# Kernel tuning notes

Measured on AMD Instinct MI355X. Metric: run time of the kernel, lower is better.

The kernel has to match this reference:

```python
import jax, jax.numpy as jnp
import numpy as np

N = 50000
E = 800000
NODE_DIM = 15
HID = 64
HEADS = 4
NEG_SLOPE = 0.2


def _add_self_loops(edge_index, n):
    loops = jnp.arange(n, dtype=edge_index.dtype)
    src = jnp.concatenate([edge_index[0], loops])
    dst = jnp.concatenate([edge_index[1], loops])
    return src, dst


def gat_conv(x, edge_index, W, att_src, att_dst, bias, concat):
    # x: [N, F_in]; W: [F_in, heads*out]; att_*: [heads, out]; bias: [heads*out] or [out]
    n = x.shape[0]
    heads, out_dim = att_src.shape
    src, dst = _add_self_loops(edge_index, n)
    h = (x @ W).reshape(n, heads, out_dim)              # [N, H, D]
    a_src = jnp.sum(h * att_src[None], axis=-1)          # [N, H]
    a_dst = jnp.sum(h * att_dst[None], axis=-1)          # [N, H]
    e = a_src[src] + a_dst[dst]                          # [E', H]
    e = jnp.where(e > 0, e, NEG_SLOPE * e)               # LeakyReLU(0.2)
    # segment softmax over incoming edges of each dst node
    m = jax.ops.segment_max(e, dst, num_segments=n)      # [N, H]
    m = jnp.where(jnp.isfinite(m), m, 0.0)
    w = jnp.exp(e - m[dst])                              # [E', H]
    z = jax.ops.segment_sum(w, dst, num_segments=n)      # [N, H]
    alpha = w / z[dst]                                   # [E', H]
    msg = alpha[:, :, None] * h[src]                     # [E', H, D]
    out = jax.ops.segment_sum(msg, dst, num_segments=n)  # [N, H, D]
    if concat:
        return out.reshape(n, heads * out_dim) + bias
    return out.mean(axis=1) + bias


def setup_inputs() -> dict:
    key = jax.random.key(0)
    ks = jax.random.split(key, 11)
    x = jax.random.normal(ks[0], (N, NODE_DIM), dtype=jnp.float32)
    edge_index = jax.random.randint(ks[1], (2, E), 0, N, dtype=jnp.int64)
    s1 = 1.0 / np.sqrt(NODE_DIM)
    s2 = 1.0 / np.sqrt(HEADS * HID)
    return {
        "x": x,
        "edge_index": edge_index,
        "W1": jax.random.normal(ks[2], (NODE_DIM, HEADS * HID), dtype=jnp.float32) * s1,
        "att_src1": jax.random.normal(ks[3], (HEADS, HID), dtype=jnp.float32) * s2,
        "att_dst1": jax.random.normal(ks[4], (HEADS, HID), dtype=jnp.float32) * s2,
        "b1": jnp.zeros((HEADS * HID,), dtype=jnp.float32),
        "W2": jax.random.normal(ks[5], (HEADS * HID, HID), dtype=jnp.float32) * s2,
        "att_src2": jax.random.normal(ks[6], (1, HID), dtype=jnp.float32) * s2,
        "att_dst2": jax.random.normal(ks[7], (1, HID), dtype=jnp.float32) * s2,
        "b2": jnp.zeros((HID,), dtype=jnp.float32),
    }


def reference(x, edge_index, W1, att_src1, att_dst1, b1, W2, att_src2, att_dst2, b2):
    h = gat_conv(x, edge_index, W1, att_src1, att_dst1, b1, concat=True)   # [N, 256]
    h = jax.nn.elu(h)
    # dropout p=0.2 skipped (eval mode)
    h = gat_conv(h, edge_index, W2, att_src2, att_dst2, b2, concat=True)   # heads=1 -> [N, 64]
    return h.mean(axis=0)                                                   # [64]
```

## Files before the change

kernel.cpp:

```cpp
#include <hip/hip_runtime.h>
#include <hip/hip_fp16.h>

#define NNODES 50000
#define NEDGES 800000
#define NEG_SLOPE 0.2f
#define NTOT (NEDGES + NNODES)
#define NB_NODE ((NNODES + 255) / 256)
#define CHUNK 4096
#define NCHUNK ((NEDGES + CHUNK - 1) / CHUNK)
#define CAPB 4800
#define CNTSTRIDE 16
#define ZPAD (NTOT + 32)

typedef _Float16 half8 __attribute__((ext_vector_type(8)));
typedef _Float16 half4 __attribute__((ext_vector_type(4)));
typedef float f32x4 __attribute__((ext_vector_type(4)));

__global__ void setup_scatter(const float* __restrict__ x, const float* __restrict__ W1,
                              const float* __restrict__ att_src, const float* __restrict__ att_dst,
                              const float* __restrict__ W2,
                              const int* __restrict__ srcs, const int* __restrict__ dsts,
                              int* __restrict__ bucket_cnt, int* __restrict__ bucketbuf,
                              float* __restrict__ x16, float* __restrict__ asrc4,
                              float* __restrict__ adst4, _Float16* __restrict__ W2T) {
    int t = threadIdx.x;
    __shared__ unsigned short meta[CHUNK];
    __shared__ int lcnt[NB_NODE], lbase[NB_NODE];
    __shared__ float swa[16][4], swd[16][4];
    if (blockIdx.x < NCHUNK) {
        int b = blockIdx.x;
        for (int i = t; i < NB_NODE; i += 256) lcnt[i] = 0;
        __syncthreads();
        int e0 = b * CHUNK;
        int e1 = e0 + CHUNK; if (e1 > NEDGES) e1 = NEDGES;
        for (int e = e0 + t; e < e1; e += 256) {
            int d = dsts[e];
            meta[e - e0] = (unsigned short)d;
            atomicAdd(&lcnt[d >> 8], 1);
        }
        __syncthreads();
        for (int i = t; i < NB_NODE; i += 256) {
            int c = lcnt[i];
            lbase[i] = c ? atomicAdd(&bucket_cnt[i * CNTSTRIDE], c) : 0;
        }
        __syncthreads();
        for (int i = t; i < NB_NODE; i += 256) lcnt[i] = 0;
        __syncthreads();
        for (int e = e0 + t; e < e1; e += 256) {
            int dv = meta[e - e0];
            int bk = dv >> 8;
            int pos = lbase[bk] + atomicAdd(&lcnt[bk], 1);
            if (pos < CAPB) bucketbuf[bk * CAPB + pos] = ((dv & 255) << 16) | srcs[e];
        }
    } else {
        int b = blockIdx.x - NCHUNK;
        if (t < 128) {
            int k = (t & 63) >> 2, h = t & 3;
            float s = 0.f;
            if (k < 15) {
                const float* att = (t < 64) ? att_src : att_dst;
#pragma unroll 16
                for (int d = 0; d < 64; ++d)
                    s += W1[k * 256 + h * 64 + d] * att[h * 64 + d];
            }
            if (t < 64) swa[k][h] = s; else swd[k][h] = s;
        }
        int tid = b * 256 + t;
        if (tid < 64 * 256) {
            int n = tid >> 8, k = tid & 255;
            W2T[n * 256 + k] = (_Float16)W2[k * 64 + n];
        }
        __syncthreads();
        int nid = tid;
        if (nid < NNODES) {
            float xv[16];
#pragma unroll
            for (int k = 0; k < 15; ++k) xv[k] = x[nid * 15 + k];
            xv[15] = 0.f;
#pragma unroll
            for (int k = 0; k < 16; k += 4)
                *(float4*)(x16 + (size_t)nid * 16 + k) =
                    make_float4(xv[k], xv[k+1], xv[k+2], xv[k+3]);
            float ps[4] = {0.f, 0.f, 0.f, 0.f}, pd[4] = {0.f, 0.f, 0.f, 0.f};
#pragma unroll
            for (int k = 0; k < 15; ++k)
#pragma unroll
                for (int h = 0; h < 4; ++h) {
                    ps[h] += xv[k] * swa[k][h];
                    pd[h] += xv[k] * swd[k][h];
                }
            *(float4*)(asrc4 + nid * 4) = make_float4(ps[0], ps[1], ps[2], ps[3]);
            *(float4*)(adst4 + nid * 4) = make_float4(pd[0], pd[1], pd[2], pd[3]);
        }
    }
}

__global__ void scanA(const int* __restrict__ bucket_cnt, const int* __restrict__ bucketbuf,
                      int* __restrict__ rowstart, int* __restrict__ partials) {
    int b = blockIdx.x, t = threadIdx.x, lane = t & 63, wid = t >> 6;
    __shared__ int hist[256];
    __shared__ int ws[4];
    int i = b * 256 + t;
    hist[t] = (i < NNODES) ? 1 : 0;
    __syncthreads();
    int n = bucket_cnt[b * CNTSTRIDE]; if (n > CAPB) n = CAPB;
    const int* buf = bucketbuf + (size_t)b * CAPB;
    for (int j = t; j < n; j += 256)
        atomicAdd(&hist[buf[j] >> 16], 1);
    __syncthreads();
    int v = (i < NNODES) ? hist[t] : 0;
    int incl = v;
#pragma unroll
    for (int off = 1; off < 64; off <<= 1) {
        int u = __shfl_up(incl, off, 64);
        if (lane >= off) incl += u;
    }
    if (lane == 63) ws[wid] = incl;
    __syncthreads();
    int w0 = ws[0], w1 = ws[1], w2 = ws[2], w3 = ws[3];
    int woff = (wid > 0 ? w0 : 0) + (wid > 1 ? w1 : 0) + (wid > 2 ? w2 : 0);
    if (i < NNODES) rowstart[i] = woff + (incl - v);
    if (t == 0) partials[b] = w0 + w1 + w2 + w3;
}

__global__ void scanB(const int* __restrict__ partials, int* __restrict__ blockoff,
                      int* __restrict__ rowstart, int nb) {
    int t = threadIdx.x, lane = t & 63, wid = t >> 6;
    int v = (t < nb) ? partials[t] : 0;
    int incl = v;
#pragma unroll
    for (int off = 1; off < 64; off <<= 1) {
        int u = __shfl_up(incl, off, 64);
        if (lane >= off) incl += u;
    }
    __shared__ int ws[4];
    if (lane == 63) ws[wid] = incl;
    __syncthreads();
    int w0 = ws[0], w1 = ws[1], w2 = ws[2], w3 = ws[3];
    int woff = (wid > 0 ? w0 : 0) + (wid > 1 ? w1 : 0) + (wid > 2 ? w2 : 0);
    if (t < nb) blockoff[t] = woff + (incl - v);
    if (t == 0) rowstart[NNODES] = w0 + w1 + w2 + w3;
}

__global__ void local_sort(const int* __restrict__ bucket_cnt, const int* __restrict__ bucketbuf,
                           int* __restrict__ rowstart, const int* __restrict__ blockoff,
                           const int* __restrict__ partials,
                           const float4* __restrict__ asrc4, const float4* __restrict__ adst4,
                           int* __restrict__ srclist, float4* __restrict__ sw4) {
    int b = blockIdx.x, t = threadIdx.x;
    __shared__ int cur[256];
    __shared__ int local[8192];
    __shared__ float4 sadst[256];
    if (b == 0 && t == 0) sw4[ZPAD] = make_float4(0.f, 0.f, 0.f, 0.f);
    int boff = blockoff[b];
    int base = rowstart[b * 256] + boff;
    int idx = b * 256 + t;
    int fin = (idx < NNODES) ? rowstart[idx] + boff : 0;
    cur[t] = (idx < NNODES) ? (fin - base) : 0;
    int nid = idx;
    if (nid < NNODES) sadst[t] = adst4[nid];
    __syncthreads();
    if (nid < NNODES) rowstart[nid] = fin;
    if (nid < NNODES) {
        int pos = atomicAdd(&cur[t], 1);
        local[pos] = (t << 16) | nid;
    }
    int n = bucket_cnt[b * CNTSTRIDE]; if (n > CAPB) n = CAPB;
    const int* buf = bucketbuf + (size_t)b * CAPB;
    for (int i = t; i < n; i += 256) {
        int entry = buf[i];
        int pos = atomicAdd(&cur[entry >> 16], 1);
        local[pos] = entry;
    }
    __syncthreads();
    int total = partials[b];
    for (int i = t; i < total; i += 256) {
        int e = local[i];
        int s = e & 0xFFFF, dl = e >> 16;
        srclist[base + i] = s;
        float4 as = asrc4[s];
        float4 ad = sadst[dl];
        float e0 = as.x + ad.x, e1 = as.y + ad.y, e2 = as.z + ad.z, e3 = as.w + ad.w;
        e0 = fmaxf(e0, NEG_SLOPE * e0); e1 = fmaxf(e1, NEG_SLOPE * e1);
        e2 = fmaxf(e2, NEG_SLOPE * e2); e3 = fmaxf(e3, NEG_SLOPE * e3);
        sw4[base + i] = make_float4(__expf(e0), __expf(e1), __expf(e2), __expf(e3));
    }
}

__global__ void layer1_aggr(const float* __restrict__ x16, const int* __restrict__ rowstart,
                            const int* __restrict__ srclist, const float4* __restrict__ sw4,
                            const float* __restrict__ W1, const float* __restrict__ b1,
                            __half* __restrict__ out1) {
    int wid = threadIdx.x >> 6, lane = threadIdx.x & 63;
    int g = lane >> 4, k = lane & 15;
    int base = blockIdx.x * 16 + wid * 4;
    int nid = base + g;
    int beg = rowstart[nid];
    int cnt = rowstart[nid + 1] - beg;
    int cmax = cnt;
    cmax = max(cmax, __shfl_xor(cmax, 16, 64));
    cmax = max(cmax, __shfl_xor(cmax, 32, 64));
    cmax = __builtin_amdgcn_readfirstlane(cmax);
    int gb = g * 16;
    float4 acc = {0.f, 0.f, 0.f, 0.f};
    float4 zs  = {0.f, 0.f, 0.f, 0.f};
    for (int c0 = 0; c0 < cmax; c0 += 16) {
        int sv = (c0 + k < cnt) ? srclist[beg + c0 + k] : 0;
        int bmax = cmax - c0; if (bmax > 16) bmax = 16;
        for (int j = 0; j < bmax; j += 4) {
            int i0 = c0 + j;
            int s0 = __shfl(sv, gb + j + 0, 64);
            int s1 = __shfl(sv, gb + j + 1, 64);
            int s2 = __shfl(sv, gb + j + 2, 64);
            int s3 = __shfl(sv, gb + j + 3, 64);
            int w0i = (i0 + 0 < cnt) ? beg + i0 + 0 : ZPAD;
            int w1i = (i0 + 1 < cnt) ? beg + i0 + 1 : ZPAD;
            int w2i = (i0 + 2 < cnt) ? beg + i0 + 2 : ZPAD;
            int w3i = (i0 + 3 < cnt) ? beg + i0 + 3 : ZPAD;
            float4 w0 = sw4[w0i];
            float4 w1 = sw4[w1i];
            float4 w2 = sw4[w2i];
            float4 w3 = sw4[w3i];
            float x0 = x16[s0 * 16 + k];
            float x1 = x16[s1 * 16 + k];
            float x2 = x16[s2 * 16 + k];
            float x3 = x16[s3 * 16 + k];
            zs.x += (w0.x + w1.x) + (w2.x + w3.x);
            zs.y += (w0.y + w1.y) + (w2.y + w3.y);
            zs.z += (w0.z + w1.z) + (w2.z + w3.z);
            zs.w += (w0.w + w1.w) + (w2.w + w3.w);
            acc.x = fmaf(w3.x, x3, fmaf(w2.x, x2, fmaf(w1.x, x1, fmaf(w0.x, x0, acc.x))));
            acc.y = fmaf(w3.y, x3, fmaf(w2.y, x2, fmaf(w1.y, x1, fmaf(w0.y, x0, acc.y))));
            acc.z = fmaf(w3.z, x3, fmaf(w2.z, x2, fmaf(w1.z, x1, fmaf(w0.z, x0, acc.z))));
            acc.w = fmaf(w3.w, x3, fmaf(w2.w, x2, fmaf(w1.w, x1, fmaf(w0.w, x0, acc.w))));
        }
    }
    __shared__ float sacc[4][4][64];
    sacc[wid][g][0 * 16 + k] = acc.x / zs.x;
    sacc[wid][g][1 * 16 + k] = acc.y / zs.y;
    sacc[wid][g][2 * 16 + k] = acc.z / zs.z;
    sacc[wid][g][3 * 16 + k] = acc.w / zs.w;
    int c = lane, h2 = c >> 4;
    float4 bo = *(const float4*)(b1 + c * 4);
    float4 o0 = bo, o1 = bo, o2 = bo, o3 = bo;
#pragma unroll
    for (int kk = 0; kk < 15; ++kk) {
        float4 wv = *(const float4*)(W1 + kk * 256 + c * 4);
        float a0 = sacc[wid][0][h2 * 16 + kk];
        float a1 = sacc[wid][1][h2 * 16 + kk];
        float a2 = sacc[wid][2][h2 * 16 + kk];
        float a3 = sacc[wid][3][h2 * 16 + kk];
        o0.x = fmaf(a0, wv.x, o0.x); o0.y = fmaf(a0, wv.y, o0.y);
        o0.z = fmaf(a0, wv.z, o0.z); o0.w = fmaf(a0, wv.w, o0.w);
        o1.x = fmaf(a1, wv.x, o1.x); o1.y = fmaf(a1, wv.y, o1.y);
        o1.z = fmaf(a1, wv.z, o1.z); o1.w = fmaf(a1, wv.w, o1.w);
        o2.x = fmaf(a2, wv.x, o2.x); o2.y = fmaf(a2, wv.y, o2.y);
        o2.z = fmaf(a2, wv.z, o2.z); o2.w = fmaf(a2, wv.w, o2.w);
        o3.x = fmaf(a3, wv.x, o3.x); o3.y = fmaf(a3, wv.y, o3.y);
        o3.z = fmaf(a3, wv.z, o3.z); o3.w = fmaf(a3, wv.w, o3.w);
    }
    float4 ov[4] = {o0, o1, o2, o3};
#pragma unroll
    for (int gp = 0; gp < 4; ++gp) {
        float p0 = ov[gp].x, p1 = ov[gp].y, p2 = ov[gp].z, p3 = ov[gp].w;
        p0 = p0 > 0.f ? p0 : __expf(p0) - 1.f;
        p1 = p1 > 0.f ? p1 : __expf(p1) - 1.f;
        p2 = p2 > 0.f ? p2 : __expf(p2) - 1.f;
        p3 = p3 > 0.f ? p3 : __expf(p3) - 1.f;
        half4 st;
        st[0] = (_Float16)p0; st[1] = (_Float16)p1;
        st[2] = (_Float16)p2; st[3] = (_Float16)p3;
        *(half4*)((_Float16*)out1 + (size_t)(base + gp) * 256 + c * 4) = st;
    }
}


__global__ __launch_bounds__(256) void layer2_gemm(const __half* __restrict__ out1,
                                                   const _Float16* __restrict__ W2T,
                                                   __half* __restrict__ h2,
                                                   const float* __restrict__ att_src2,
                                                   const float* __restrict__ att_dst2,
                                                   float* __restrict__ as2,
                                                   float* __restrict__ ad2) {
    int w = threadIdx.x >> 6, lane = threadIdx.x & 63;
    int m16 = lane & 15, quad = lane >> 4;
    int r0 = blockIdx.x * 64 + w * 16;
    const _Float16* A = (const _Float16*)out1;
    f32x4 acc[4] = {{0.f,0.f,0.f,0.f},{0.f,0.f,0.f,0.f},{0.f,0.f,0.f,0.f},{0.f,0.f,0.f,0.f}};
    int row = r0 + m16; if (row >= NNODES) row = NNODES - 1;
#pragma unroll
    for (int k0 = 0; k0 < 256; k0 += 32) {
        half8 a = *(const half8*)(A + (size_t)row * 256 + k0 + quad * 8);
#pragma unroll
        for (int nt = 0; nt < 4; ++nt) {
            half8 b = *(const half8*)(W2T + (size_t)(nt * 16 + m16) * 256 + k0 + quad * 8);
            acc[nt] = __builtin_amdgcn_mfma_f32_16x16x32_f16(a, b, acc[nt], 0, 0, 0);
        }
    }
    __shared__ _Float16 tile[64][72];
#pragma unroll
    for (int nt = 0; nt < 4; ++nt)
#pragma unroll
        for (int r = 0; r < 4; ++r)
            tile[w * 16 + quad * 4 + r][nt * 16 + m16] = (_Float16)acc[nt][r];
    __syncthreads();
    int t = threadIdx.x;
    int trow = t >> 2, seg = t & 3;
    int rg = blockIdx.x * 64 + trow;
    if (rg < NNODES) {
        float4 v0 = *(float4*)&tile[trow][seg * 16];
        float4 v1 = *(float4*)&tile[trow][seg * 16 + 8];
        _Float16* dst = (_Float16*)h2 + (size_t)rg * 64 + seg * 16;
        *(float4*)dst = v0;
        *(float4*)(dst + 8) = v1;
        const _Float16* hv = &tile[trow][seg * 16];
        float ps = 0.f, pd = 0.f;
#pragma unroll
        for (int j = 0; j < 16; ++j) {
            float v = (float)hv[j];
            ps += v * att_src2[seg * 16 + j];
            pd += v * att_dst2[seg * 16 + j];
        }
        ps += __shfl_xor(ps, 1, 64); ps += __shfl_xor(ps, 2, 64);
        pd += __shfl_xor(pd, 1, 64); pd += __shfl_xor(pd, 2, 64);
        if (seg == 0) { as2[rg] = ps; ad2[rg] = pd; }
    }
}

__global__ void layer2_aggr(const __half* __restrict__ h2, const int* __restrict__ rowstart,
                            const int* __restrict__ srclist,
                            const float* __restrict__ as2, const float* __restrict__ ad2,
                            const float* __restrict__ b2, float* __restrict__ out2) {
    int wid = threadIdx.x >> 6, lane = threadIdx.x & 63;
    int sub = lane >> 5, l2 = lane & 31;
    int nid = blockIdx.x * 8 + wid * 2 + sub;
    int beg = rowstart[nid];
    int cnt = rowstart[nid + 1] - beg;
    int cmax = max(cnt, __shfl_xor(cnt, 32, 64));
    cmax = __builtin_amdgcn_readfirstlane(cmax);
    float ad = ad2[nid];
    const __half2* hp = (const __half2*)h2;
    __half2 acc2 = __float2half2_rn(0.f);
    float zs = 0.f;
    int sb = sub * 32;
    for (int c0 = 0; c0 < cmax; c0 += 32) {
        int sv = (c0 + l2 < cnt) ? srclist[beg + c0 + l2] : 0;
        int bmax = cmax - c0; if (bmax > 32) bmax = 32;
        for (int j = 0; j < bmax; j += 4) {
#pragma unroll
            for (int u = 0; u < 4; ++u) {
                int jj = j + u;
                int s = __shfl(sv, sb + jj, 64);
                bool valid = (c0 + jj) < cnt;
                float e = as2[s] + ad;
                e = fmaxf(e, NEG_SLOPE * e);
                float wv = valid ? __expf(e) : 0.f;
                __half2 gv = hp[s * 32 + l2];
                zs += wv;
                acc2 = __hfma2(__float2half2_rn(wv), gv, acc2);
            }
        }
    }
    float2 f = __half22float2(acc2);
    float rz = 1.f / zs;
    float2 bo = *(const float2*)(b2 + l2 * 2);
    *(float2*)(out2 + (size_t)nid * 64 + l2 * 2) = make_float2(f.x * rz + bo.x,
                                                               f.y * rz + bo.y);
}


__global__ void reduce_kernel(const float* __restrict__ out2, float* __restrict__ dout) {
    int t = threadIdx.x;
    int col = t & 63, sub = t >> 6;
    float acc = 0.f;
    for (int r = blockIdx.x * 4 + sub; r < NNODES; r += 256 * 4)
        acc += out2[r * 64 + col];
    __shared__ float sh[256];
    sh[t] = acc;
    __syncthreads();
    if (t < 64) {
        float v = sh[t] + sh[t + 64] + sh[t + 128] + sh[t + 192];
        atomicAdd(&dout[t], v * (1.0f / NNODES));
    }
}


extern "C" void kernel_launch(void* const* d_in, const int* in_sizes, int n_in,
                              void* d_out, int out_size, void* d_ws, size_t ws_size,
                              hipStream_t stream) {
    const float* x        = (const float*)d_in[0];
    const int*   ei       = (const int*)d_in[1];
    const float* W1       = (const float*)d_in[2];
    const float* att_src1 = (const float*)d_in[3];
    const float* att_dst1 = (const float*)d_in[4];
    const float* b1       = (const float*)d_in[5];
    const float* W2       = (const float*)d_in[6];
    const float* att_src2 = (const float*)d_in[7];
    const float* att_dst2 = (const float*)d_in[8];
    const float* b2       = (const float*)d_in[9];
    float* out = (float*)d_out;

    char* ws = (char*)d_ws;
    size_t off = 0;
    auto take = [&](size_t bytes) -> char* {
        char* p = ws + off;
        off = (off + bytes + 255) & ~(size_t)255;
        return p;
    };
    int*      bucket_cnt = (int*)take((size_t)NB_NODE * CNTSTRIDE * sizeof(int));
    int*      bucketbuf  = (int*)take((size_t)NB_NODE * CAPB * sizeof(int));
    int*      rowstart   = (int*)take((NNODES + 1) * sizeof(int));
    int*      partials   = (int*)take(256 * sizeof(int));
    int*      blockoff   = (int*)take(256 * sizeof(int));
    int*      srclist    = (int*)take(((size_t)NTOT + 64) * sizeof(int));
    float*    sw4        = (float*)take(((size_t)NTOT + 64) * 4 * sizeof(float));
    float*    x16        = (float*)take((size_t)NNODES * 16 * sizeof(float));
    float*    asrc4      = (float*)take((size_t)NNODES * 4 * sizeof(float));
    float*    adst4      = (float*)take((size_t)NNODES * 4 * sizeof(float));
    __half*   out1       = (__half*)take((size_t)NNODES * 256 * sizeof(__half));
    _Float16* W2T        = (_Float16*)take(64 * 256 * sizeof(_Float16));
    __half*   h2         = (__half*)take((size_t)NNODES * 64 * sizeof(__half));
    float*    as2        = (float*)take((size_t)NNODES * sizeof(float));
    float*    ad2        = (float*)take((size_t)NNODES * sizeof(float));
    float*    out2       = (float*)take((size_t)NNODES * 64 * sizeof(float));

    const int* srcs = ei;
    const int* dsts = ei + NEDGES;

    hipMemsetAsync(d_out, 0, 64 * sizeof(float), stream);
    hipMemsetAsync(bucket_cnt, 0, (size_t)NB_NODE * CNTSTRIDE * sizeof(int), stream);

    setup_scatter<<<NCHUNK + NB_NODE, 256, 0, stream>>>(x, W1, att_src1, att_dst1, W2,
                                                        srcs, dsts, bucket_cnt, bucketbuf,
                                                        x16, asrc4, adst4, W2T);
    scanA<<<NB_NODE, 256, 0, stream>>>(bucket_cnt, bucketbuf, rowstart, partials);
    scanB<<<1, 256, 0, stream>>>(partials, blockoff, rowstart, NB_NODE);
    local_sort<<<NB_NODE, 256, 0, stream>>>(bucket_cnt, bucketbuf, rowstart, blockoff, partials,
                                            (const float4*)asrc4, (const float4*)adst4,
                                            srclist, (float4*)sw4);

    layer1_aggr<<<NNODES / 16, 256, 0, stream>>>(x16, rowstart, srclist, (const float4*)sw4,
                                                 W1, b1, out1);

    layer2_gemm<<<(NNODES + 63) / 64, 256, 0, stream>>>(out1, W2T, h2, att_src2, att_dst2,
                                                        as2, ad2);
    layer2_aggr<<<NNODES / 8, 256, 0, stream>>>(h2, rowstart, srclist, as2, ad2, b2, out2);

    reduce_kernel<<<256, 256, 0, stream>>>(out2, out);
}
```

Baseline: 204.2 us.

## Fuse layer-2 GEMM into layer-1 aggregation and fold block scan into local sort

The layer-1 aggregation kernel now keeps its 16-row fp16 output tile in shared memory and runs the layer-2 MFMA projection and attention dot products directly, so the N×256 fp16 intermediate is no longer written to and reread from global memory. The separate single-block scanB launch is removed; each local_sort block instead sums the partials of the blocks before it with shared atomics, and the last block writes the total row count. This saves one launch and a large round trip through global memory. In exchange it adds redundant per-block partial sums, extra block-wide barriers and larger shared-memory use in the fused kernel.

```diff
diff --git a/kernel.cpp b/kernel.cpp
--- a/kernel.cpp
+++ b/kernel.cpp
@@ -123,44 +123,36 @@
     if (t == 0) partials[b] = w0 + w1 + w2 + w3;
 }
 
-__global__ void scanB(const int* __restrict__ partials, int* __restrict__ blockoff,
-                      int* __restrict__ rowstart, int nb) {
-    int t = threadIdx.x, lane = t & 63, wid = t >> 6;
-    int v = (t < nb) ? partials[t] : 0;
-    int incl = v;
-#pragma unroll
-    for (int off = 1; off < 64; off <<= 1) {
-        int u = __shfl_up(incl, off, 64);
-        if (lane >= off) incl += u;
-    }
-    __shared__ int ws[4];
-    if (lane == 63) ws[wid] = incl;
-    __syncthreads();
-    int w0 = ws[0], w1 = ws[1], w2 = ws[2], w3 = ws[3];
-    int woff = (wid > 0 ? w0 : 0) + (wid > 1 ? w1 : 0) + (wid > 2 ? w2 : 0);
-    if (t < nb) blockoff[t] = woff + (incl - v);
-    if (t == 0) rowstart[NNODES] = w0 + w1 + w2 + w3;
-}
-
 __global__ void local_sort(const int* __restrict__ bucket_cnt, const int* __restrict__ bucketbuf,
-                           int* __restrict__ rowstart, const int* __restrict__ blockoff,
-                           const int* __restrict__ partials,
+                           int* __restrict__ rowstart, const int* __restrict__ partials,
                            const float4* __restrict__ asrc4, const float4* __restrict__ adst4,
                            int* __restrict__ srclist, float4* __restrict__ sw4) {
     int b = blockIdx.x, t = threadIdx.x;
     __shared__ int cur[256];
     __shared__ int local[8192];
     __shared__ float4 sadst[256];
+    __shared__ int boffs[2];
+    if (t < 2) boffs[t] = 0;
+    int idx = b * 256 + t;
+    int nid = idx;
+    int rs0 = rowstart[b * 256];
+    int fin0 = (idx < NNODES) ? rowstart[idx] : 0;
+    if (nid < NNODES) sadst[t] = adst4[nid];
+    __syncthreads();
+    if (t < NB_NODE) {
+        int v = partials[t];
+        if (t < b) atomicAdd(&boffs[0], v);
+        atomicAdd(&boffs[1], v);
+    }
     if (b == 0 && t == 0) sw4[ZPAD] = make_float4(0.f, 0.f, 0.f, 0.f);
-    int boff = blockoff[b];
-    int base = rowstart[b * 256] + boff;
-    int idx = b * 256 + t;
-    int fin = (idx < NNODES) ? rowstart[idx] + boff : 0;
+    __syncthreads();
+    int boff = boffs[0];
+    int base = rs0 + boff;
+    int fin = fin0 + boff;
     cur[t] = (idx < NNODES) ? (fin - base) : 0;
-    int nid = idx;
-    if (nid < NNODES) sadst[t] = adst4[nid];
     __syncthreads();
     if (nid < NNODES) rowstart[nid] = fin;
+    if (b == NB_NODE - 1 && t == 0) rowstart[NNODES] = boffs[1];
     if (nid < NNODES) {
         int pos = atomicAdd(&cur[t], 1);
         local[pos] = (t << 16) | nid;
@@ -187,10 +179,13 @@
     }
 }
 
-__global__ void layer1_aggr(const float* __restrict__ x16, const int* __restrict__ rowstart,
-                            const int* __restrict__ srclist, const float4* __restrict__ sw4,
-                            const float* __restrict__ W1, const float* __restrict__ b1,
-                            __half* __restrict__ out1) {
+__global__ __launch_bounds__(256) void layer1_fused(
+        const float* __restrict__ x16, const int* __restrict__ rowstart,
+        const int* __restrict__ srclist, const float4* __restrict__ sw4,
+        const float* __restrict__ W1, const float* __restrict__ b1,
+        const _Float16* __restrict__ W2T,
+        const float* __restrict__ att_src2, const float* __restrict__ att_dst2,
+        __half* __restrict__ h2, float* __restrict__ as2, float* __restrict__ ad2) {
     int wid = threadIdx.x >> 6, lane = threadIdx.x & 63;
     int g = lane >> 4, k = lane & 15;
     int base = blockIdx.x * 16 + wid * 4;
@@ -240,16 +235,16 @@
     sacc[wid][g][1 * 16 + k] = acc.y / zs.y;
     sacc[wid][g][2 * 16 + k] = acc.z / zs.z;
     sacc[wid][g][3 * 16 + k] = acc.w / zs.w;
-    int c = lane, h2 = c >> 4;
+    int c = lane, h2i = c >> 4;
     float4 bo = *(const float4*)(b1 + c * 4);
     float4 o0 = bo, o1 = bo, o2 = bo, o3 = bo;
 #pragma unroll
     for (int kk = 0; kk < 15; ++kk) {
         float4 wv = *(const float4*)(W1 + kk * 256 + c * 4);
-        float a0 = sacc[wid][0][h2 * 16 + kk];
-        float a1 = sacc[wid][1][h2 * 16 + kk];
-        float a2 = sacc[wid][2][h2 * 16 + kk];
-        float a3 = sacc[wid][3][h2 * 16 + kk];
+        float a0 = sacc[wid][0][h2i * 16 + kk];
+        float a1 = sacc[wid][1][h2i * 16 + kk];
+        float a2 = sacc[wid][2][h2i * 16 + kk];
+        float a3 = sacc[wid][3][h2i * 16 + kk];
         o0.x = fmaf(a0, wv.x, o0.x); o0.y = fmaf(a0, wv.y, o0.y);
         o0.z = fmaf(a0, wv.z, o0.z); o0.w = fmaf(a0, wv.w, o0.w);
         o1.x = fmaf(a1, wv.x, o1.x); o1.y = fmaf(a1, wv.y, o1.y);
@@ -259,6 +254,7 @@
         o3.x = fmaf(a3, wv.x, o3.x); o3.y = fmaf(a3, wv.y, o3.y);
         o3.z = fmaf(a3, wv.z, o3.z); o3.w = fmaf(a3, wv.w, o3.w);
     }
+    __shared__ _Float16 ot[16][264];
     float4 ov[4] = {o0, o1, o2, o3};
 #pragma unroll
     for (int gp = 0; gp < 4; ++gp) {
@@ -270,61 +266,38 @@
         half4 st;
         st[0] = (_Float16)p0; st[1] = (_Float16)p1;
         st[2] = (_Float16)p2; st[3] = (_Float16)p3;
-        *(half4*)((_Float16*)out1 + (size_t)(base + gp) * 256 + c * 4) = st;
-    }
-}
-
-
-__global__ __launch_bounds__(256) void layer2_gemm(const __half* __restrict__ out1,
-                                                   const _Float16* __restrict__ W2T,
-                                                   __half* __restrict__ h2,
-                                                   const float* __restrict__ att_src2,
-                                                   const float* __restrict__ att_dst2,
-                                                   float* __restrict__ as2,
-                                                   float* __restrict__ ad2) {
-    int w = threadIdx.x >> 6, lane = threadIdx.x & 63;
+        *(half4*)&ot[wid * 4 + gp][c * 4] = st;
+    }
+    __syncthreads();
     int m16 = lane & 15, quad = lane >> 4;
-    int r0 = blockIdx.x * 64 + w * 16;
-    const _Float16* A = (const _Float16*)out1;
-    f32x4 acc[4] = {{0.f,0.f,0.f,0.f},{0.f,0.f,0.f,0.f},{0.f,0.f,0.f,0.f},{0.f,0.f,0.f,0.f}};
-    int row = r0 + m16; if (row >= NNODES) row = NNODES - 1;
+    f32x4 cc = {0.f, 0.f, 0.f, 0.f};
 #pragma unroll
     for (int k0 = 0; k0 < 256; k0 += 32) {
-        half8 a = *(const half8*)(A + (size_t)row * 256 + k0 + quad * 8);
-#pragma unroll
-        for (int nt = 0; nt < 4; ++nt) {
-            half8 b = *(const half8*)(W2T + (size_t)(nt * 16 + m16) * 256 + k0 + quad * 8);
-            acc[nt] = __builtin_amdgcn_mfma_f32_16x16x32_f16(a, b, acc[nt], 0, 0, 0);
-        }
-    }
-    __shared__ _Float16 tile[64][72];
-#pragma unroll
-    for (int nt = 0; nt < 4; ++nt)
-#pragma unroll
-        for (int r = 0; r < 4; ++r)
-            tile[w * 16 + quad * 4 + r][nt * 16 + m16] = (_Float16)acc[nt][r];
-    __syncthreads();
-    int t = threadIdx.x;
-    int trow = t >> 2, seg = t & 3;
-    int rg = blockIdx.x * 64 + trow;
-    if (rg < NNODES) {
-        float4 v0 = *(float4*)&tile[trow][seg * 16];
-        float4 v1 = *(float4*)&tile[trow][seg * 16 + 8];
-        _Float16* dst = (_Float16*)h2 + (size_t)rg * 64 + seg * 16;
-        *(float4*)dst = v0;
-        *(float4*)(dst + 8) = v1;
-        const _Float16* hv = &tile[trow][seg * 16];
-        float ps = 0.f, pd = 0.f;
-#pragma unroll
-        for (int j = 0; j < 16; ++j) {
-            float v = (float)hv[j];
-            ps += v * att_src2[seg * 16 + j];
-            pd += v * att_dst2[seg * 16 + j];
-        }
-        ps += __shfl_xor(ps, 1, 64); ps += __shfl_xor(ps, 2, 64);
-        pd += __shfl_xor(pd, 1, 64); pd += __shfl_xor(pd, 2, 64);
-        if (seg == 0) { as2[rg] = ps; ad2[rg] = pd; }
-    }
+        half8 a = *(const half8*)&ot[m16][k0 + quad * 8];
+        half8 bf = *(const half8*)(W2T + (size_t)(wid * 16 + m16) * 256 + k0 + quad * 8);
+        cc = __builtin_amdgcn_mfma_f32_16x16x32_f16(a, bf, cc, 0, 0, 0);
+    }
+    __shared__ _Float16 h2t[16][72];
+#pragma unroll
+    for (int r = 0; r < 4; ++r)
+        h2t[quad * 4 + r][wid * 16 + m16] = (_Float16)cc[r];
+    __syncthreads();
+    int trow = threadIdx.x >> 4, tc = threadIdx.x & 15;
+    int rg = blockIdx.x * 16 + trow;
+    half4 hval = *(const half4*)&h2t[trow][tc * 4];
+    *(half4*)((_Float16*)h2 + (size_t)rg * 64 + tc * 4) = hval;
+    float ps = 0.f, pd = 0.f;
+#pragma unroll
+    for (int j = 0; j < 4; ++j) {
+        float v = (float)hval[j];
+        ps += v * att_src2[tc * 4 + j];
+        pd += v * att_dst2[tc * 4 + j];
+    }
+    ps += __shfl_xor(ps, 1, 64); ps += __shfl_xor(ps, 2, 64);
+    ps += __shfl_xor(ps, 4, 64); ps += __shfl_xor(ps, 8, 64);
+    pd += __shfl_xor(pd, 1, 64); pd += __shfl_xor(pd, 2, 64);
+    pd += __shfl_xor(pd, 4, 64); pd += __shfl_xor(pd, 8, 64);
+    if (tc == 0) { as2[rg] = ps; ad2[rg] = pd; }
 }
 
 __global__ void layer2_aggr(const __half* __restrict__ h2, const int* __restrict__ rowstart,
@@ -411,13 +384,11 @@
     int*      bucketbuf  = (int*)take((size_t)NB_NODE * CAPB * sizeof(int));
     int*      rowstart   = (int*)take((NNODES + 1) * sizeof(int));
     int*      partials   = (int*)take(256 * sizeof(int));
-    int*      blockoff   = (int*)take(256 * sizeof(int));
     int*      srclist    = (int*)take(((size_t)NTOT + 64) * sizeof(int));
     float*    sw4        = (float*)take(((size_t)NTOT + 64) * 4 * sizeof(float));
     float*    x16        = (float*)take((size_t)NNODES * 16 * sizeof(float));
     float*    asrc4      = (float*)take((size_t)NNODES * 4 * sizeof(float));
     float*    adst4      = (float*)take((size_t)NNODES * 4 * sizeof(float));
-    __half*   out1       = (__half*)take((size_t)NNODES * 256 * sizeof(__half));
     _Float16* W2T        = (_Float16*)take(64 * 256 * sizeof(_Float16));
     __half*   h2         = (__half*)take((size_t)NNODES * 64 * sizeof(__half));
     float*    as2        = (float*)take((size_t)NNODES * sizeof(float));
@@ -434,16 +405,14 @@
                                                         srcs, dsts, bucket_cnt, bucketbuf,
                                                         x16, asrc4, adst4, W2T);
     scanA<<<NB_NODE, 256, 0, stream>>>(bucket_cnt, bucketbuf, rowstart, partials);
-    scanB<<<1, 256, 0, stream>>>(partials, blockoff, rowstart, NB_NODE);
-    local_sort<<<NB_NODE, 256, 0, stream>>>(bucket_cnt, bucketbuf, rowstart, blockoff, partials,
+    local_sort<<<NB_NODE, 256, 0, stream>>>(bucket_cnt, bucketbuf, rowstart, partials,
                                             (const float4*)asrc4, (const float4*)adst4,
                                             srclist, (float4*)sw4);
 
-    layer1_aggr<<<NNODES / 16, 256, 0, stream>>>(x16, rowstart, srclist, (const float4*)sw4,
-                                                 W1, b1, out1);
-
-    layer2_gemm<<<(NNODES + 63) / 64, 256, 0, stream>>>(out1, W2T, h2, att_src2, att_dst2,
-                                                        as2, ad2);
+    layer1_fused<<<NNODES / 16, 256, 0, stream>>>(x16, rowstart, srclist, (const float4*)sw4,
+                                                  W1, b1, W2T, att_src2, att_dst2,
+                                                  h2, as2, ad2);
+
     layer2_aggr<<<NNODES / 8, 256, 0, stream>>>(h2, rowstart, srclist, as2, ad2, b2, out2);
 
     reduce_kernel<<<256, 256, 0, stream>>>(out2, out);
```

Measured after the change: 192.7 us. 5.6% less time.
